# Kernel optimization log

Measured on AMD Instinct MI355X. Metric: run time of the kernel, lower is better.

## Reference

```python
import jax, jax.numpy as jnp
import numpy as np

OBS_LEN = 20
PRED_LEN = 30
NUM_MODES = 6
DATA_DIM = 2
DROPOUT_P = 0.25
NEG_SLOPE = 0.01
H_DIM = 256
B = 8192


def setup_inputs() -> dict:
    key = jax.random.key(0)
    ks = jax.random.split(key, 20)
    s = 0.05
    inp = {
        "traj_abs": jax.random.normal(ks[0], (OBS_LEN, B, DATA_DIM), jnp.float32),
        "traj_rel": jax.random.normal(ks[1], (OBS_LEN, B, DATA_DIM), jnp.float32),
        "state_h": jax.random.normal(ks[2], (1, B, H_DIM), jnp.float32),
        "c0": jax.random.normal(ks[3], (NUM_MODES, B, H_DIM), jnp.float32),
        # spatial embedding Linear(40, 40)
        "W_se": jax.random.normal(ks[4], (OBS_LEN * 2, OBS_LEN * 2), jnp.float32) * s,
        "b_se": jax.random.normal(ks[5], (OBS_LEN * 2,), jnp.float32) * s,
        # LSTM weights: input 40 -> hidden 256, gates order i,f,g,o
        "W_ih": jax.random.normal(ks[6], (4 * H_DIM, OBS_LEN * 2), jnp.float32) * s,
        "W_hh": jax.random.normal(ks[7], (4 * H_DIM, H_DIM), jnp.float32) * s,
        "b_ih": jax.random.normal(ks[8], (4 * H_DIM,), jnp.float32) * s,
        "b_hh": jax.random.normal(ks[9], (4 * H_DIM,), jnp.float32) * s,
        # per-mode prediction heads Linear(256, 2)
        "W_pred": jax.random.normal(ks[10], (NUM_MODES, DATA_DIM, H_DIM), jnp.float32) * s,
        "b_pred": jax.random.normal(ks[11], (NUM_MODES, DATA_DIM), jnp.float32) * s,
        # confidence PredictionNet (norm=False), latent = PRED_LEN*DATA_DIM = 60
        "pn_w1": jax.random.normal(ks[12], (PRED_LEN * DATA_DIM, PRED_LEN * DATA_DIM), jnp.float32) * s,
        "pn_b1": jax.random.normal(ks[13], (PRED_LEN * DATA_DIM,), jnp.float32) * s,
        "pn_w2": jax.random.normal(ks[14], (PRED_LEN * DATA_DIM, PRED_LEN * DATA_DIM), jnp.float32) * s,
        "pn_b2": jax.random.normal(ks[15], (PRED_LEN * DATA_DIM,), jnp.float32) * s,
        "pn_wfc": jax.random.normal(ks[16], (1, PRED_LEN * DATA_DIM), jnp.float32) * s,
        "pn_bfc": jax.random.normal(ks[17], (1,), jnp.float32) * s,
    }
    return inp


def _decode(traj_rel, state_h, c0, W_se, b_se, W_ih, W_hh, b_ih, b_hh,
            W_pred, b_pred, pn_w1, pn_b1, pn_w2, pn_b2, pn_wfc, pn_bfc):
    batch = traj_rel.shape[1]
    h0 = state_h[0]  # (B, H)
    keep = 1.0 - DROPOUT_P
    # one dropout key per (mode, step); deterministic stand-in for torch dropout
    keys = jax.random.split(jax.random.key(42), NUM_MODES * PRED_LEN).reshape(NUM_MODES, PRED_LEN)

    def one_mode(Wp, bp, c0m, keys_m):
        def step(carry, key):
            h, c, buf = carry  # buf: (OBS_LEN, B, 2) rolling window of rel displacements
            x = buf.transpose(1, 0, 2).reshape(batch, -1) @ W_se.T + b_se  # (B, 40)
            x = jnp.where(x > 0, x, NEG_SLOPE * x)  # leaky_relu
            mask = jax.random.bernoulli(key, keep, x.shape)
            x = jnp.where(mask, x / keep, 0.0)  # dropout (training=True)
            gates = x @ W_ih.T + b_ih + h @ W_hh.T + b_hh  # (B, 4H)
            i, f, g, o = jnp.split(gates, 4, axis=-1)
            c = jax.nn.sigmoid(f) * c + jax.nn.sigmoid(i) * jnp.tanh(g)
            h = jax.nn.sigmoid(o) * jnp.tanh(c)
            rel = h @ Wp.T + bp  # (B, 2)
            buf = jnp.roll(buf, -1, axis=0).at[-1].set(rel)
            return (h, c, buf), rel

        _, rels = jax.lax.scan(step, (h0, c0m, traj_rel), keys_m)
        return rels  # (PRED_LEN, B, 2)

    rels = jax.vmap(one_mode)(W_pred, b_pred, c0, keys)  # (M, T, B, 2)
    pred = rels.transpose(2, 0, 1, 3)  # (B, M, T, 2)

    # confidence PredictionNet (norm=False)
    x = pred.reshape(batch, NUM_MODES, PRED_LEN * DATA_DIM)
    y = jax.nn.relu(x @ pn_w1.T + pn_b1)
    y = jax.nn.relu(y @ pn_w2.T + pn_b2 + x)
    conf = (y @ pn_wfc.T + pn_bfc).reshape(batch, NUM_MODES)
    conf = jax.nn.softmax(conf, axis=1)
    return pred, conf


def reference(traj_abs, traj_rel, state_h, c0, W_se, b_se, W_ih, W_hh, b_ih, b_hh,
              W_pred, b_pred, pn_w1, pn_b1, pn_w2, pn_b2, pn_wfc, pn_bfc):
    # traj_abs unused in the 'Latent' branch (only its shape is read)
    return _decode(traj_rel, state_h, c0, W_se, b_se, W_ih, W_hh, b_ih, b_hh,
                   W_pred, b_pred, pn_w1, pn_b1, pn_w2, pn_b2, pn_wfc, pn_bfc)
```

## Files before the change

### kernel.cpp

```cpp
#include <hip/hip_runtime.h>
#include <cstdint>

#define JAX_PARTITIONABLE 1

#define OBS_LEN 20
#define PRED_LEN 30
#define NUM_MODES 6
#define BATCH 8192
#define H 256
#define MB (NUM_MODES * BATCH)
#define KPAD 320

typedef __attribute__((ext_vector_type(8))) short bf16x8;
typedef __attribute__((ext_vector_type(4))) float f32x4;

__host__ __device__ inline void tf2x32(uint32_t k0, uint32_t k1, uint32_t c0, uint32_t c1,
                                       uint32_t& o0, uint32_t& o1) {
  uint32_t ks0 = k0, ks1 = k1, ks2 = k0 ^ k1 ^ 0x1BD11BDAu;
  uint32_t x0 = c0 + ks0, x1 = c1 + ks1;
#define TF_R(x, r) (((x) << (r)) | ((x) >> (32 - (r))))
#define TF_RND(r)  { x0 += x1; x1 = TF_R(x1, r); x1 ^= x0; }
  TF_RND(13) TF_RND(15) TF_RND(26) TF_RND(6)   x0 += ks1; x1 += ks2 + 1u;
  TF_RND(17) TF_RND(29) TF_RND(16) TF_RND(24)  x0 += ks2; x1 += ks0 + 2u;
  TF_RND(13) TF_RND(15) TF_RND(26) TF_RND(6)   x0 += ks0; x1 += ks1 + 3u;
  TF_RND(17) TF_RND(29) TF_RND(16) TF_RND(24)  x0 += ks1; x1 += ks2 + 4u;
  TF_RND(13) TF_RND(15) TF_RND(26) TF_RND(6)   x0 += ks2; x1 += ks0 + 5u;
  o0 = x0; o1 = x1;
#undef TF_RND
#undef TF_R
}

__device__ inline void step_key(int m, int t, uint32_t& k0, uint32_t& k1) {
#if JAX_PARTITIONABLE
  tf2x32(0u, 42u, 0u, (uint32_t)(m * PRED_LEN + t), k0, k1);
#else
  int i = m * PRED_LEN + t;
  int n0 = 2 * i, n1 = 2 * i + 1;
  uint32_t a0, a1;
  if (n0 < 180) { tf2x32(0u, 42u, (uint32_t)n0, (uint32_t)(n0 + 180), a0, a1); k0 = a0; }
  else          { tf2x32(0u, 42u, (uint32_t)(n0 - 180), (uint32_t)n0, a0, a1); k0 = a1; }
  if (n1 < 180) { tf2x32(0u, 42u, (uint32_t)n1, (uint32_t)(n1 + 180), a0, a1); k1 = a0; }
  else          { tf2x32(0u, 42u, (uint32_t)(n1 - 180), (uint32_t)n1, a0, a1); k1 = a1; }
#endif
}

__device__ inline uint32_t mask_bits(uint32_t k0, uint32_t k1, uint32_t n) {
#if JAX_PARTITIONABLE
  uint32_t o0, o1;
  tf2x32(k0, k1, 0u, n, o0, o1);
  return o0 ^ o1;
#else
  const uint32_t HALF = (uint32_t)(BATCH * 40 / 2);
  uint32_t o0, o1;
  if (n < HALF) { tf2x32(k0, k1, n, n + HALF, o0, o1); return o0; }
  else          { tf2x32(k0, k1, n - HALF, n, o0, o1); return o1; }
#endif
}

__device__ __forceinline__ float sigf(float x) { return 1.0f / (1.0f + __expf(-x)); }
__device__ __forceinline__ float tanhfast(float x) {
  float e = __expf(-2.0f * fabsf(x));
  float t = (1.0f - e) / (1.0f + e);
  return x >= 0.f ? t : -t;
}
__device__ __forceinline__ ushort f2bf(float f) {
  uint32_t u = __float_as_uint(f);
  uint32_t r = (u + 0x7fffu + ((u >> 16) & 1u)) >> 16;
  return (ushort)r;
}
__device__ __forceinline__ float bf2f(uint32_t u) { return __uint_as_float(u << 16); }

__global__ __launch_bounds__(256) void k_prep(const float* __restrict__ Wih, const float* __restrict__ Whh,
                                              const float* __restrict__ bih, const float* __restrict__ bhh,
                                              ushort* __restrict__ WTb, float* __restrict__ bias) {
  int idx = blockIdx.x * 256 + threadIdx.x;
  if (idx < 1024 * KPAD) {
    int np = idx / KPAD, k = idx - np * KPAD;
    int cg = np >> 7, r = np & 127;
    int nt = r >> 4, col = r & 15;
    int N = (nt & 3) * 256 + cg * 32 + (nt >> 2) * 16 + col;
    float v = (k < 40) ? Wih[N * 40 + k] : (k < 296 ? Whh[N * 256 + (k - 40)] : 0.f);
    WTb[idx] = f2bf(v);
  }
  if (idx < 1024) bias[idx] = bih[idx] + bhh[idx];
}

__global__ __launch_bounds__(256) void k_init(const float* __restrict__ state_h, const float* __restrict__ c0,
                                              float* __restrict__ cst, ushort* __restrict__ Ab0,
                                              ushort* __restrict__ Ab1) {
  int idx = blockIdx.x * 256 + threadIdx.x;
  if (idx < MB * 64) {
    int row = idx >> 6;
    int j4 = (idx & 63) << 2;
    float4 cv = *(const float4*)(c0 + (size_t)idx * 4);
    *(float4*)(cst + (size_t)idx * 4) = cv;
    int b = row & (BATCH - 1);
    float4 hv = *(const float4*)(state_h + (size_t)b * H + j4);
    ushort4 hb = {f2bf(hv.x), f2bf(hv.y), f2bf(hv.z), f2bf(hv.w)};
    *(ushort4*)(Ab0 + (size_t)row * KPAD + 40 + j4) = hb;
  }
  if (idx < MB * 6) {
    int row = idx / 6, p4 = (idx - row * 6) << 2;
    ushort4 z = {0, 0, 0, 0};
    *(ushort4*)(Ab0 + (size_t)row * KPAD + 296 + p4) = z;
    *(ushort4*)(Ab1 + (size_t)row * KPAD + 296 + p4) = z;
  }
}

__global__ __launch_bounds__(256) void k_embed(const float* __restrict__ traj_rel, const float* __restrict__ rels,
                                               const float* __restrict__ Wse, const float* __restrict__ bse,
                                               ushort* __restrict__ Ax, int t) {
  __shared__ float sW[1600];
  __shared__ float sb[40];
  int tid = threadIdx.x;
  for (int i = tid; i < 1600; i += 256) sW[i] = Wse[i];
  if (tid < 40) sb[tid] = bse[tid];
  __syncthreads();
  int gid = blockIdx.x * 256 + tid;
  int b = gid & (BATCH - 1);
  int m = gid >> 13;
  float win[40];
#pragma unroll
  for (int kk = 0; kk < OBS_LEN; kk++) {
    int st = t + kk;
    const float* p = (st < OBS_LEN)
        ? (traj_rel + (((size_t)st * BATCH + b) << 1))
        : (rels + (((size_t)(m * PRED_LEN + (st - OBS_LEN)) * BATCH + b) << 1));
    float2 w = *(const float2*)p;
    win[kk * 2] = w.x; win[kk * 2 + 1] = w.y;
  }
  uint32_t k0, k1;
  step_key(m, t, k0, k1);
  uint32_t nb = (uint32_t)(b * 40);
  ushort* orow = Ax + (size_t)gid * KPAD;
#pragma unroll
  for (int jo = 0; jo < 5; jo++) {
    uint32_t pk[4];
#pragma unroll
    for (int jp = 0; jp < 4; jp++) {
      ushort lo = 0, hi = 0;
#pragma unroll
      for (int ji = 0; ji < 2; ji++) {
        int j = jo * 8 + jp * 2 + ji;
        float a = sb[j];
#pragma unroll
        for (int p = 0; p < 40; p += 4) {
          float4 w = *(const float4*)&sW[j * 40 + p];
          a = fmaf(win[p + 3], w.w, fmaf(win[p + 2], w.z, fmaf(win[p + 1], w.y, fmaf(win[p], w.x, a))));
        }
        a = a > 0.f ? a : 0.01f * a;
        uint32_t bits = mask_bits(k0, k1, nb + (uint32_t)j);
        float u = __uint_as_float((bits >> 9) | 0x3f800000u) - 1.0f;
        ushort r = (u < 0.75f) ? f2bf(a * 1.3333333730697632f) : (ushort)0;
        if (ji == 0) lo = r; else hi = r;
      }
      pk[jp] = (uint32_t)lo | ((uint32_t)hi << 16);
    }
    uint4 v = {pk[0], pk[1], pk[2], pk[3]};
    *(uint4*)(orow + jo * 8) = v;
  }
}

__global__ __launch_bounds__(256) void k_gates(const ushort* __restrict__ Ain, const ushort* __restrict__ WTb,
                                               const float* __restrict__ bias, float* __restrict__ cst,
                                               ushort* __restrict__ Anext) {
  __shared__ __align__(16) ushort lA[2][128][40];
  __shared__ __align__(16) ushort lB[2][128][40];
  int tid = threadIdx.x;
  int w = tid >> 6, lane = tid & 63;
  int row0 = blockIdx.x * 128;
  int cg = blockIdx.y;
  int sr = tid >> 1, sh = (tid & 1) << 4;
  const ushort* gA = Ain + (size_t)(row0 + sr) * KPAD + sh;
  const ushort* gB = WTb + (size_t)(cg * 128 + sr) * KPAD + sh;

  f32x4 zero = {0.f, 0.f, 0.f, 0.f};
  f32x4 acc[2][8];
#pragma unroll
  for (int i = 0; i < 2; i++)
#pragma unroll
    for (int j = 0; j < 8; j++) acc[i][j] = zero;

  uint4 ra0 = *(const uint4*)gA;
  uint4 ra1 = *(const uint4*)(gA + 8);
  uint4 rb0 = *(const uint4*)gB;
  uint4 rb1 = *(const uint4*)(gB + 8);
  *(uint4*)&lA[0][sr][sh] = ra0;
  *(uint4*)&lA[0][sr][sh + 8] = ra1;
  *(uint4*)&lB[0][sr][sh] = rb0;
  *(uint4*)&lB[0][sr][sh + 8] = rb1;
  __syncthreads();

  int fm = lane & 15, fq = lane >> 4;
  for (int kt = 0; kt < 10; kt++) {
    int cur = kt & 1;
    if (kt < 9) {
      ra0 = *(const uint4*)(gA + (kt + 1) * 32);
      ra1 = *(const uint4*)(gA + (kt + 1) * 32 + 8);
      rb0 = *(const uint4*)(gB + (kt + 1) * 32);
      rb1 = *(const uint4*)(gB + (kt + 1) * 32 + 8);
    }
    bf16x8 af[2], bfr[8];
#pragma unroll
    for (int rt = 0; rt < 2; rt++) af[rt] = *(const bf16x8*)&lA[cur][w * 32 + rt * 16 + fm][fq * 8];
#pragma unroll
    for (int nt = 0; nt < 8; nt++) bfr[nt] = *(const bf16x8*)&lB[cur][nt * 16 + fm][fq * 8];
#pragma unroll
    for (int rt = 0; rt < 2; rt++)
#pragma unroll
      for (int nt = 0; nt < 8; nt++)
        acc[rt][nt] = __builtin_amdgcn_mfma_f32_16x16x32_bf16(af[rt], bfr[nt], acc[rt][nt], 0, 0, 0);
    if (kt < 9) {
      *(uint4*)&lA[cur ^ 1][sr][sh] = ra0;
      *(uint4*)&lA[cur ^ 1][sr][sh + 8] = ra1;
      *(uint4*)&lB[cur ^ 1][sr][sh] = rb0;
      *(uint4*)&lB[cur ^ 1][sr][sh + 8] = rb1;
      __syncthreads();
    }
  }

#pragma unroll
  for (int jg = 0; jg < 2; jg++) {
    int jh = cg * 32 + jg * 16 + fm;
    float bi = bias[jh], bfg = bias[256 + jh], bg = bias[512 + jh], bo = bias[768 + jh];
#pragma unroll
    for (int rt = 0; rt < 2; rt++) {
#pragma unroll
      for (int reg = 0; reg < 4; reg++) {
        int row = row0 + w * 32 + rt * 16 + fq * 4 + reg;
        float gi = acc[rt][jg * 4 + 0][reg] + bi;
        float gf = acc[rt][jg * 4 + 1][reg] + bfg;
        float gg = acc[rt][jg * 4 + 2][reg] + bg;
        float go = acc[rt][jg * 4 + 3][reg] + bo;
        size_t ci = (size_t)row * H + jh;
        float cv = cst[ci];
        float c2 = sigf(gf) * cv + sigf(gi) * tanhfast(gg);
        cst[ci] = c2;
        float hn = sigf(go) * tanhfast(c2);
        Anext[(size_t)row * KPAD + 40 + jh] = f2bf(hn);
      }
    }
  }
}

__global__ __launch_bounds__(256) void k_pred(const ushort* __restrict__ hsrc, const float* __restrict__ Wp,
                                              const float* __restrict__ bp, float* __restrict__ rels, int t) {
  int tid = threadIdx.x;
  int wv = tid >> 6, lane = tid & 63;
  int grp = lane >> 3, lg = lane & 7;
  int row = blockIdx.x * 32 + wv * 8 + grp;
  int m = row / BATCH, b = row & (BATCH - 1);
  const ushort* hr = hsrc + (size_t)row * KPAD + 40 + lg * 32;
  const float* w0 = Wp + m * 512 + lg * 32;
  const float* w1 = w0 + 256;
  float s0 = 0.f, s1 = 0.f;
#pragma unroll
  for (int q = 0; q < 4; q++) {
    uint4 hv = *(const uint4*)(hr + q * 8);
    float h0 = bf2f(hv.x & 0xffffu), h1 = bf2f(hv.x >> 16);
    float h2 = bf2f(hv.y & 0xffffu), h3 = bf2f(hv.y >> 16);
    float h4 = bf2f(hv.z & 0xffffu), h5 = bf2f(hv.z >> 16);
    float h6 = bf2f(hv.w & 0xffffu), h7 = bf2f(hv.w >> 16);
    float4 wa0 = *(const float4*)(w0 + q * 8);
    float4 wa1 = *(const float4*)(w0 + q * 8 + 4);
    float4 wb0 = *(const float4*)(w1 + q * 8);
    float4 wb1 = *(const float4*)(w1 + q * 8 + 4);
    s0 += h0 * wa0.x + h1 * wa0.y + h2 * wa0.z + h3 * wa0.w
        + h4 * wa1.x + h5 * wa1.y + h6 * wa1.z + h7 * wa1.w;
    s1 += h0 * wb0.x + h1 * wb0.y + h2 * wb0.z + h3 * wb0.w
        + h4 * wb1.x + h5 * wb1.y + h6 * wb1.z + h7 * wb1.w;
  }
#pragma unroll
  for (int off = 1; off < 8; off <<= 1) {
    s0 += __shfl_xor(s0, off, 64);
    s1 += __shfl_xor(s1, off, 64);
  }
  if (lg == 0) {
    float2 r = make_float2(s0 + bp[m * 2], s1 + bp[m * 2 + 1]);
    *(float2*)(rels + ((size_t)(m * PRED_LEN + t) * BATCH + b) * 2) = r;
  }
}

__global__ __launch_bounds__(256) void k_transconf(const float* __restrict__ rels,
                                                   const float* __restrict__ W1, const float* __restrict__ b1,
                                                   const float* __restrict__ W2, const float* __restrict__ b2,
                                                   const float* __restrict__ wfc, const float* __restrict__ bfc,
                                                   float* __restrict__ out) {
  __shared__ float tile[32][361];
  __shared__ float sW1[3600];
  __shared__ float sW2[3600];
  __shared__ float sb1[60], sb2[60], swfc[60];
  __shared__ float sy1[192][61];
  __shared__ float slg[32][6];
  int tid = threadIdx.x;
  for (int i = tid; i < 3600; i += 256) { sW1[i] = W1[i]; sW2[i] = W2[i]; }
  if (tid < 60) { sb1[tid] = b1[tid]; sb2[tid] = b2[tid]; swfc[tid] = wfc[tid]; }
  int b0 = blockIdx.x * 32;
  for (int i = tid; i < 11520; i += 256) {
    int bl = i & 31, c = i >> 5;
    int mm = c / 60, r = c % 60;
    tile[bl][c] = rels[((size_t)((mm * PRED_LEN + (r >> 1)) * BATCH) + (b0 + bl)) * 2 + (r & 1)];
  }
  __syncthreads();
  for (int i = tid; i < 11520; i += 256) {
    int bl = i / 360, c = i % 360;
    out[(size_t)(b0 + bl) * 360 + c] = tile[bl][c];
  }
  if (tid < 192) {
    int bl = tid / 6, mm = tid - bl * 6;
    int xb = mm * 60;
    for (int q = 0; q < 60; q++) {
      float acl = sb1[q];
#pragma unroll
      for (int p = 0; p < 60; p++) acl = fmaf(tile[bl][xb + p], sW1[q * 60 + p], acl);
      sy1[tid][q] = fmaxf(acl, 0.f);
    }
    float logit = bfc[0];
    for (int q = 0; q < 60; q++) {
      float acl = sb2[q] + tile[bl][xb + q];
#pragma unroll
      for (int p = 0; p < 60; p++) acl = fmaf(sy1[tid][p], sW2[q * 60 + p], acl);
      logit = fmaf(fmaxf(acl, 0.f), swfc[q], logit);
    }
    slg[bl][mm] = logit;
  }
  __syncthreads();
  if (tid < 32) {
    float mx = slg[tid][0];
#pragma unroll
    for (int m = 1; m < 6; m++) mx = fmaxf(mx, slg[tid][m]);
    float e[6], s = 0.f;
#pragma unroll
    for (int m = 0; m < 6; m++) { e[m] = __expf(slg[tid][m] - mx); s += e[m]; }
    float inv = 1.0f / s;
    size_t base = (size_t)BATCH * 360 + (size_t)(b0 + tid) * 6;
#pragma unroll
    for (int m = 0; m < 6; m++) out[base + m] = e[m] * inv;
  }
}

extern "C" void kernel_launch(void* const* d_in, const int* in_sizes, int n_in,
                              void* d_out, int out_size, void* d_ws, size_t ws_size,
                              hipStream_t stream) {
  const float* traj_rel = (const float*)d_in[1];
  const float* state_h  = (const float*)d_in[2];
  const float* c0       = (const float*)d_in[3];
  const float* Wse      = (const float*)d_in[4];
  const float* bse      = (const float*)d_in[5];
  const float* Wih      = (const float*)d_in[6];
  const float* Whh      = (const float*)d_in[7];
  const float* bih      = (const float*)d_in[8];
  const float* bhh      = (const float*)d_in[9];
  const float* Wp       = (const float*)d_in[10];
  const float* bp       = (const float*)d_in[11];
  const float* W1       = (const float*)d_in[12];
  const float* b1       = (const float*)d_in[13];
  const float* W2       = (const float*)d_in[14];
  const float* b2       = (const float*)d_in[15];
  const float* wfc      = (const float*)d_in[16];
  const float* bfc      = (const float*)d_in[17];
  float* out = (float*)d_out;

  float* cst  = (float*)d_ws;
  float* rels = cst + (size_t)MB * H;
  float* bias = rels + (size_t)NUM_MODES * PRED_LEN * BATCH * 2;
  ushort* WTb = (ushort*)(bias + 1024);
  ushort* Ab0 = WTb + (size_t)1024 * KPAD;
  ushort* Ab1 = Ab0 + (size_t)MB * KPAD;

  k_prep<<<1280, 256, 0, stream>>>(Wih, Whh, bih, bhh, WTb, bias);
  k_init<<<12288, 256, 0, stream>>>(state_h, c0, cst, Ab0, Ab1);
  for (int t = 0; t < PRED_LEN; t++) {
    ushort* Acur  = (t & 1) ? Ab1 : Ab0;
    ushort* Anext = (t & 1) ? Ab0 : Ab1;
    k_embed<<<192, 256, 0, stream>>>(traj_rel, rels, Wse, bse, Acur, t);
    k_gates<<<dim3(384, 8), 256, 0, stream>>>(Acur, WTb, bias, cst, Anext);
    k_pred<<<1536, 256, 0, stream>>>(Anext, Wp, bp, rels, t);
  }
  k_transconf<<<256, 256, 0, stream>>>(rels, W1, b1, W2, b2, wfc, bfc, out);
}
```

Baseline: 3.525 ms.

## Fuse whole 30-step LSTM decode into one persistent kernel with on-chip state

Replaces the per-step embed/gates/pred launches (90 launches) with one kernel where each block owns 64 rows of one mode and loops over all 30 steps. Cell state stays in registers, hidden state and the input window stay in LDS, and the gate GEMM uses 32x32x16 bf16 MFMA with weights pre-swizzled and streamed from global/L2 each step. This removes the global round-trips of h, c and the A matrix plus launch overhead. In exchange it depends on occupancy of 768 blocks of 512 threads with large register/LDS use, and re-reads the full weight matrix per block per step from cache.

```diff
diff --git a/kernel.cpp b/kernel.cpp
--- a/kernel.cpp
+++ b/kernel.cpp
@@ -9,10 +9,9 @@
 #define BATCH 8192
 #define H 256
 #define MB (NUM_MODES * BATCH)
-#define KPAD 320
 
 typedef __attribute__((ext_vector_type(8))) short bf16x8;
-typedef __attribute__((ext_vector_type(4))) float f32x4;
+typedef __attribute__((ext_vector_type(16))) float f32x16;
 
 __host__ __device__ inline void tf2x32(uint32_t k0, uint32_t k1, uint32_t c0, uint32_t c1,
                                        uint32_t& o0, uint32_t& o1) {
@@ -71,213 +70,198 @@
 __device__ __forceinline__ float bf2f(uint32_t u) { return __uint_as_float(u << 16); }
 
 __global__ __launch_bounds__(256) void k_prep(const float* __restrict__ Wih, const float* __restrict__ Whh,
-                                              const float* __restrict__ bih, const float* __restrict__ bhh,
-                                              ushort* __restrict__ WTb, float* __restrict__ bias) {
+                                              ushort* __restrict__ W2) {
   int idx = blockIdx.x * 256 + threadIdx.x;
-  if (idx < 1024 * KPAD) {
-    int np = idx / KPAD, k = idx - np * KPAD;
-    int cg = np >> 7, r = np & 127;
-    int nt = r >> 4, col = r & 15;
-    int N = (nt & 3) * 256 + cg * 32 + (nt >> 2) * 16 + col;
+  if (idx < 20 * 8 * 4 * 2 * 32 * 8) {
+    int j = idx & 7, n = (idx >> 3) & 31, kh = (idx >> 8) & 1;
+    int g = (idx >> 9) & 3, w = (idx >> 11) & 7, kt = idx >> 14;
+    int N = g * 256 + w * 32 + n;
+    int k = kt * 16 + kh * 8 + j;
     float v = (k < 40) ? Wih[N * 40 + k] : (k < 296 ? Whh[N * 256 + (k - 40)] : 0.f);
-    WTb[idx] = f2bf(v);
-  }
-  if (idx < 1024) bias[idx] = bih[idx] + bhh[idx];
-}
-
-__global__ __launch_bounds__(256) void k_init(const float* __restrict__ state_h, const float* __restrict__ c0,
-                                              float* __restrict__ cst, ushort* __restrict__ Ab0,
-                                              ushort* __restrict__ Ab1) {
-  int idx = blockIdx.x * 256 + threadIdx.x;
-  if (idx < MB * 64) {
-    int row = idx >> 6;
-    int j4 = (idx & 63) << 2;
-    float4 cv = *(const float4*)(c0 + (size_t)idx * 4);
-    *(float4*)(cst + (size_t)idx * 4) = cv;
-    int b = row & (BATCH - 1);
-    float4 hv = *(const float4*)(state_h + (size_t)b * H + j4);
-    ushort4 hb = {f2bf(hv.x), f2bf(hv.y), f2bf(hv.z), f2bf(hv.w)};
-    *(ushort4*)(Ab0 + (size_t)row * KPAD + 40 + j4) = hb;
-  }
-  if (idx < MB * 6) {
-    int row = idx / 6, p4 = (idx - row * 6) << 2;
-    ushort4 z = {0, 0, 0, 0};
-    *(ushort4*)(Ab0 + (size_t)row * KPAD + 296 + p4) = z;
-    *(ushort4*)(Ab1 + (size_t)row * KPAD + 296 + p4) = z;
-  }
-}
-
-__global__ __launch_bounds__(256) void k_embed(const float* __restrict__ traj_rel, const float* __restrict__ rels,
-                                               const float* __restrict__ Wse, const float* __restrict__ bse,
-                                               ushort* __restrict__ Ax, int t) {
-  __shared__ float sW[1600];
-  __shared__ float sb[40];
+    W2[idx] = f2bf(v);
+  }
+}
+
+__global__ __launch_bounds__(512, 2) void k_decode(
+    const float* __restrict__ traj_rel, const float* __restrict__ state_h,
+    const float* __restrict__ c0, const float* __restrict__ Wse, const float* __restrict__ bse,
+    const float* __restrict__ bih, const float* __restrict__ bhh,
+    const ushort* __restrict__ W2, const float* __restrict__ Wp, const float* __restrict__ bp,
+    float* __restrict__ rels) {
+  __shared__ __align__(16) ushort sA[64][328];
+  __shared__ float sWse[1600];
+  __shared__ float sWp[512];
+  __shared__ float sbse[40];
+  __shared__ float swin[64][40];
+
   int tid = threadIdx.x;
-  for (int i = tid; i < 1600; i += 256) sW[i] = Wse[i];
-  if (tid < 40) sb[tid] = bse[tid];
+  int w = tid >> 6, lane = tid & 63;
+  int khl = lane >> 5, col = lane & 31;
+  int blk = blockIdx.x;
+  int m = blk >> 7;
+  int b0 = (blk & 127) * 64;
+  int jh = w * 32 + col;
+
+  for (int i = tid; i < 1600; i += 512) sWse[i] = Wse[i];
+  if (tid < 512) sWp[tid] = Wp[m * 512 + tid];
+  if (tid < 40) sbse[tid] = bse[tid];
+  for (int i = tid; i < 64 * 20; i += 512) {
+    int row = i / 20, kk = i - row * 20;
+    float2 v = *(const float2*)(traj_rel + ((size_t)kk * BATCH + b0 + row) * 2);
+    swin[row][kk * 2] = v.x; swin[row][kk * 2 + 1] = v.y;
+  }
+  for (int i = tid; i < 64 * 256; i += 512) {
+    int row = i >> 8, j = i & 255;
+    sA[row][40 + j] = f2bf(state_h[((size_t)(b0 + row)) * 256 + j]);
+  }
+  for (int i = tid; i < 64 * 32; i += 512) {
+    int row = i >> 5;
+    sA[row][296 + (i & 31)] = 0;
+  }
+  float rbi = bih[jh] + bhh[jh];
+  float rbf = bih[256 + jh] + bhh[256 + jh];
+  float rbg = bih[512 + jh] + bhh[512 + jh];
+  float rbo = bih[768 + jh] + bhh[768 + jh];
+  float creg[2][16];
+#pragma unroll
+  for (int rt = 0; rt < 2; rt++)
+#pragma unroll
+    for (int reg = 0; reg < 16; reg++) {
+      int row = rt * 32 + (reg & 3) + 8 * (reg >> 2) + 4 * khl;
+      creg[rt][reg] = c0[((size_t)m * BATCH + b0 + row) * H + jh];
+    }
+  float bpx = bp[m * 2], bpy = bp[m * 2 + 1];
   __syncthreads();
-  int gid = blockIdx.x * 256 + tid;
-  int b = gid & (BATCH - 1);
-  int m = gid >> 13;
-  float win[40];
-#pragma unroll
-  for (int kk = 0; kk < OBS_LEN; kk++) {
-    int st = t + kk;
-    const float* p = (st < OBS_LEN)
-        ? (traj_rel + (((size_t)st * BATCH + b) << 1))
-        : (rels + (((size_t)(m * PRED_LEN + (st - OBS_LEN)) * BATCH + b) << 1));
-    float2 w = *(const float2*)p;
-    win[kk * 2] = w.x; win[kk * 2 + 1] = w.y;
-  }
-  uint32_t k0, k1;
-  step_key(m, t, k0, k1);
-  uint32_t nb = (uint32_t)(b * 40);
-  ushort* orow = Ax + (size_t)gid * KPAD;
-#pragma unroll
-  for (int jo = 0; jo < 5; jo++) {
-    uint32_t pk[4];
-#pragma unroll
-    for (int jp = 0; jp < 4; jp++) {
-      ushort lo = 0, hi = 0;
-#pragma unroll
-      for (int ji = 0; ji < 2; ji++) {
-        int j = jo * 8 + jp * 2 + ji;
-        float a = sb[j];
+
+  int q = tid & 7, prow = tid >> 3;
+  const int jb0 = q * 32;
+
+#pragma unroll 1
+  for (int t = 0; t < PRED_LEN; t++) {
+    if (t > 0) {
+      float s0 = 0.f, s1 = 0.f;
+#pragma unroll
+      for (int p = 0; p < 4; p++) {
+        uint4 hv = *(const uint4*)&sA[prow][40 + jb0 + p * 8];
+        float hh[8] = {bf2f(hv.x & 0xffffu), bf2f(hv.x >> 16), bf2f(hv.y & 0xffffu), bf2f(hv.y >> 16),
+                       bf2f(hv.z & 0xffffu), bf2f(hv.z >> 16), bf2f(hv.w & 0xffffu), bf2f(hv.w >> 16)};
+#pragma unroll
+        for (int e = 0; e < 8; e++) {
+          s0 = fmaf(hh[e], sWp[jb0 + p * 8 + e], s0);
+          s1 = fmaf(hh[e], sWp[256 + jb0 + p * 8 + e], s1);
+        }
+      }
+#pragma unroll
+      for (int off = 1; off < 8; off <<= 1) {
+        s0 += __shfl_xor(s0, off, 64);
+        s1 += __shfl_xor(s1, off, 64);
+      }
+      if (q == 0) {
+        float rx = s0 + bpx, ry = s1 + bpy;
+        *(float2*)(rels + ((size_t)(m * PRED_LEN + (t - 1)) * BATCH + b0 + prow) * 2) =
+            make_float2(rx, ry);
+        int slot = (t - 1) % 20;
+        swin[prow][slot * 2] = rx; swin[prow][slot * 2 + 1] = ry;
+      }
+    }
+    {
+      uint32_t k0, k1;
+      step_key(m, t, k0, k1);
+      float win[40];
+#pragma unroll
+      for (int kk = 0; kk < 20; kk++) {
+        int idx = t + kk;
+        if (idx >= 40) idx -= 40; else if (idx >= 20) idx -= 20;
+        win[kk * 2] = swin[prow][idx * 2];
+        win[kk * 2 + 1] = swin[prow][idx * 2 + 1];
+      }
+      uint32_t nb = (uint32_t)((b0 + prow) * 40 + q * 5);
+#pragma unroll
+      for (int jj = 0; jj < 5; jj++) {
+        int j = q * 5 + jj;
+        float a = sbse[j];
 #pragma unroll
         for (int p = 0; p < 40; p += 4) {
-          float4 w = *(const float4*)&sW[j * 40 + p];
-          a = fmaf(win[p + 3], w.w, fmaf(win[p + 2], w.z, fmaf(win[p + 1], w.y, fmaf(win[p], w.x, a))));
+          float4 wv = *(const float4*)&sWse[j * 40 + p];
+          a = fmaf(win[p + 3], wv.w, fmaf(win[p + 2], wv.z, fmaf(win[p + 1], wv.y, fmaf(win[p], wv.x, a))));
         }
         a = a > 0.f ? a : 0.01f * a;
-        uint32_t bits = mask_bits(k0, k1, nb + (uint32_t)j);
+        uint32_t bits = mask_bits(k0, k1, nb + (uint32_t)jj);
         float u = __uint_as_float((bits >> 9) | 0x3f800000u) - 1.0f;
-        ushort r = (u < 0.75f) ? f2bf(a * 1.3333333730697632f) : (ushort)0;
-        if (ji == 0) lo = r; else hi = r;
-      }
-      pk[jp] = (uint32_t)lo | ((uint32_t)hi << 16);
-    }
-    uint4 v = {pk[0], pk[1], pk[2], pk[3]};
-    *(uint4*)(orow + jo * 8) = v;
-  }
-}
-
-__global__ __launch_bounds__(256) void k_gates(const ushort* __restrict__ Ain, const ushort* __restrict__ WTb,
-                                               const float* __restrict__ bias, float* __restrict__ cst,
-                                               ushort* __restrict__ Anext) {
-  __shared__ __align__(16) ushort lA[2][128][40];
-  __shared__ __align__(16) ushort lB[2][128][40];
-  int tid = threadIdx.x;
-  int w = tid >> 6, lane = tid & 63;
-  int row0 = blockIdx.x * 128;
-  int cg = blockIdx.y;
-  int sr = tid >> 1, sh = (tid & 1) << 4;
-  const ushort* gA = Ain + (size_t)(row0 + sr) * KPAD + sh;
-  const ushort* gB = WTb + (size_t)(cg * 128 + sr) * KPAD + sh;
-
-  f32x4 zero = {0.f, 0.f, 0.f, 0.f};
-  f32x4 acc[2][8];
-#pragma unroll
-  for (int i = 0; i < 2; i++)
-#pragma unroll
-    for (int j = 0; j < 8; j++) acc[i][j] = zero;
-
-  uint4 ra0 = *(const uint4*)gA;
-  uint4 ra1 = *(const uint4*)(gA + 8);
-  uint4 rb0 = *(const uint4*)gB;
-  uint4 rb1 = *(const uint4*)(gB + 8);
-  *(uint4*)&lA[0][sr][sh] = ra0;
-  *(uint4*)&lA[0][sr][sh + 8] = ra1;
-  *(uint4*)&lB[0][sr][sh] = rb0;
-  *(uint4*)&lB[0][sr][sh + 8] = rb1;
-  __syncthreads();
-
-  int fm = lane & 15, fq = lane >> 4;
-  for (int kt = 0; kt < 10; kt++) {
-    int cur = kt & 1;
-    if (kt < 9) {
-      ra0 = *(const uint4*)(gA + (kt + 1) * 32);
-      ra1 = *(const uint4*)(gA + (kt + 1) * 32 + 8);
-      rb0 = *(const uint4*)(gB + (kt + 1) * 32);
-      rb1 = *(const uint4*)(gB + (kt + 1) * 32 + 8);
-    }
-    bf16x8 af[2], bfr[8];
-#pragma unroll
-    for (int rt = 0; rt < 2; rt++) af[rt] = *(const bf16x8*)&lA[cur][w * 32 + rt * 16 + fm][fq * 8];
-#pragma unroll
-    for (int nt = 0; nt < 8; nt++) bfr[nt] = *(const bf16x8*)&lB[cur][nt * 16 + fm][fq * 8];
+        sA[prow][j] = (u < 0.75f) ? f2bf(a * 1.3333333730697632f) : (ushort)0;
+      }
+    }
+    __syncthreads();
+
+    f32x16 acc[2][4];
 #pragma unroll
     for (int rt = 0; rt < 2; rt++)
 #pragma unroll
-      for (int nt = 0; nt < 8; nt++)
-        acc[rt][nt] = __builtin_amdgcn_mfma_f32_16x16x32_bf16(af[rt], bfr[nt], acc[rt][nt], 0, 0, 0);
-    if (kt < 9) {
-      *(uint4*)&lA[cur ^ 1][sr][sh] = ra0;
-      *(uint4*)&lA[cur ^ 1][sr][sh + 8] = ra1;
-      *(uint4*)&lB[cur ^ 1][sr][sh] = rb0;
-      *(uint4*)&lB[cur ^ 1][sr][sh + 8] = rb1;
-      __syncthreads();
-    }
-  }
-
-#pragma unroll
-  for (int jg = 0; jg < 2; jg++) {
-    int jh = cg * 32 + jg * 16 + fm;
-    float bi = bias[jh], bfg = bias[256 + jh], bg = bias[512 + jh], bo = bias[768 + jh];
-#pragma unroll
-    for (int rt = 0; rt < 2; rt++) {
-#pragma unroll
-      for (int reg = 0; reg < 4; reg++) {
-        int row = row0 + w * 32 + rt * 16 + fq * 4 + reg;
-        float gi = acc[rt][jg * 4 + 0][reg] + bi;
-        float gf = acc[rt][jg * 4 + 1][reg] + bfg;
-        float gg = acc[rt][jg * 4 + 2][reg] + bg;
-        float go = acc[rt][jg * 4 + 3][reg] + bo;
-        size_t ci = (size_t)row * H + jh;
-        float cv = cst[ci];
-        float c2 = sigf(gf) * cv + sigf(gi) * tanhfast(gg);
-        cst[ci] = c2;
-        float hn = sigf(go) * tanhfast(c2);
-        Anext[(size_t)row * KPAD + 40 + jh] = f2bf(hn);
-      }
-    }
-  }
-}
-
-__global__ __launch_bounds__(256) void k_pred(const ushort* __restrict__ hsrc, const float* __restrict__ Wp,
-                                              const float* __restrict__ bp, float* __restrict__ rels, int t) {
-  int tid = threadIdx.x;
-  int wv = tid >> 6, lane = tid & 63;
-  int grp = lane >> 3, lg = lane & 7;
-  int row = blockIdx.x * 32 + wv * 8 + grp;
-  int m = row / BATCH, b = row & (BATCH - 1);
-  const ushort* hr = hsrc + (size_t)row * KPAD + 40 + lg * 32;
-  const float* w0 = Wp + m * 512 + lg * 32;
-  const float* w1 = w0 + 256;
-  float s0 = 0.f, s1 = 0.f;
-#pragma unroll
-  for (int q = 0; q < 4; q++) {
-    uint4 hv = *(const uint4*)(hr + q * 8);
-    float h0 = bf2f(hv.x & 0xffffu), h1 = bf2f(hv.x >> 16);
-    float h2 = bf2f(hv.y & 0xffffu), h3 = bf2f(hv.y >> 16);
-    float h4 = bf2f(hv.z & 0xffffu), h5 = bf2f(hv.z >> 16);
-    float h6 = bf2f(hv.w & 0xffffu), h7 = bf2f(hv.w >> 16);
-    float4 wa0 = *(const float4*)(w0 + q * 8);
-    float4 wa1 = *(const float4*)(w0 + q * 8 + 4);
-    float4 wb0 = *(const float4*)(w1 + q * 8);
-    float4 wb1 = *(const float4*)(w1 + q * 8 + 4);
-    s0 += h0 * wa0.x + h1 * wa0.y + h2 * wa0.z + h3 * wa0.w
-        + h4 * wa1.x + h5 * wa1.y + h6 * wa1.z + h7 * wa1.w;
-    s1 += h0 * wb0.x + h1 * wb0.y + h2 * wb0.z + h3 * wb0.w
-        + h4 * wb1.x + h5 * wb1.y + h6 * wb1.z + h7 * wb1.w;
-  }
-#pragma unroll
-  for (int off = 1; off < 8; off <<= 1) {
-    s0 += __shfl_xor(s0, off, 64);
-    s1 += __shfl_xor(s1, off, 64);
-  }
-  if (lg == 0) {
-    float2 r = make_float2(s0 + bp[m * 2], s1 + bp[m * 2 + 1]);
-    *(float2*)(rels + ((size_t)(m * PRED_LEN + t) * BATCH + b) * 2) = r;
+      for (int g = 0; g < 4; g++)
+#pragma unroll
+        for (int reg = 0; reg < 16; reg++) acc[rt][g][reg] = 0.f;
+
+    const ushort* Wbase = W2 + (size_t)lane * 8;
+    bf16x8 bc[4], bn[4];
+#pragma unroll
+    for (int g = 0; g < 4; g++) bc[g] = *(const bf16x8*)(Wbase + ((0 * 8 + w) * 4 + g) * 512);
+#pragma unroll
+    for (int kt = 0; kt < 20; kt++) {
+      if (kt < 19) {
+#pragma unroll
+        for (int g = 0; g < 4; g++)
+          bn[g] = *(const bf16x8*)(Wbase + (((kt + 1) * 8 + w) * 4 + g) * 512);
+      }
+      bf16x8 a0 = *(const bf16x8*)&sA[col][kt * 16 + khl * 8];
+      bf16x8 a1 = *(const bf16x8*)&sA[32 + col][kt * 16 + khl * 8];
+#pragma unroll
+      for (int g = 0; g < 4; g++) {
+        acc[0][g] = __builtin_amdgcn_mfma_f32_32x32x16_bf16(a0, bc[g], acc[0][g], 0, 0, 0);
+        acc[1][g] = __builtin_amdgcn_mfma_f32_32x32x16_bf16(a1, bc[g], acc[1][g], 0, 0, 0);
+      }
+#pragma unroll
+      for (int g = 0; g < 4; g++) bc[g] = bn[g];
+    }
+    __syncthreads();
+
+#pragma unroll
+    for (int rt = 0; rt < 2; rt++)
+#pragma unroll
+      for (int reg = 0; reg < 16; reg++) {
+        int row = rt * 32 + (reg & 3) + 8 * (reg >> 2) + 4 * khl;
+        float gi = acc[rt][0][reg] + rbi;
+        float gf = acc[rt][1][reg] + rbf;
+        float gg = acc[rt][2][reg] + rbg;
+        float go = acc[rt][3][reg] + rbo;
+        float c2 = sigf(gf) * creg[rt][reg] + sigf(gi) * tanhfast(gg);
+        creg[rt][reg] = c2;
+        sA[row][40 + jh] = f2bf(sigf(go) * tanhfast(c2));
+      }
+    __syncthreads();
+  }
+
+  {
+    float s0 = 0.f, s1 = 0.f;
+#pragma unroll
+    for (int p = 0; p < 4; p++) {
+      uint4 hv = *(const uint4*)&sA[prow][40 + jb0 + p * 8];
+      float hh[8] = {bf2f(hv.x & 0xffffu), bf2f(hv.x >> 16), bf2f(hv.y & 0xffffu), bf2f(hv.y >> 16),
+                     bf2f(hv.z & 0xffffu), bf2f(hv.z >> 16), bf2f(hv.w & 0xffffu), bf2f(hv.w >> 16)};
+#pragma unroll
+      for (int e = 0; e < 8; e++) {
+        s0 = fmaf(hh[e], sWp[jb0 + p * 8 + e], s0);
+        s1 = fmaf(hh[e], sWp[256 + jb0 + p * 8 + e], s1);
+      }
+    }
+#pragma unroll
+    for (int off = 1; off < 8; off <<= 1) {
+      s0 += __shfl_xor(s0, off, 64);
+      s1 += __shfl_xor(s1, off, 64);
+    }
+    if (q == 0) {
+      *(float2*)(rels + ((size_t)(m * PRED_LEN + 29) * BATCH + b0 + prow) * 2) =
+          make_float2(s0 + bpx, s1 + bpy);
+    }
   }
 }
 
@@ -309,18 +293,18 @@
   if (tid < 192) {
     int bl = tid / 6, mm = tid - bl * 6;
     int xb = mm * 60;
-    for (int q = 0; q < 60; q++) {
-      float acl = sb1[q];
-#pragma unroll
-      for (int p = 0; p < 60; p++) acl = fmaf(tile[bl][xb + p], sW1[q * 60 + p], acl);
-      sy1[tid][q] = fmaxf(acl, 0.f);
+    for (int qq = 0; qq < 60; qq++) {
+      float acl = sb1[qq];
+#pragma unroll
+      for (int p = 0; p < 60; p++) acl = fmaf(tile[bl][xb + p], sW1[qq * 60 + p], acl);
+      sy1[tid][qq] = fmaxf(acl, 0.f);
     }
     float logit = bfc[0];
-    for (int q = 0; q < 60; q++) {
-      float acl = sb2[q] + tile[bl][xb + q];
-#pragma unroll
-      for (int p = 0; p < 60; p++) acl = fmaf(sy1[tid][p], sW2[q * 60 + p], acl);
-      logit = fmaf(fmaxf(acl, 0.f), swfc[q], logit);
+    for (int qq = 0; qq < 60; qq++) {
+      float acl = sb2[qq] + tile[bl][xb + qq];
+#pragma unroll
+      for (int p = 0; p < 60; p++) acl = fmaf(sy1[tid][p], sW2[qq * 60 + p], acl);
+      logit = fmaf(fmaxf(acl, 0.f), swfc[qq], logit);
     }
     slg[bl][mm] = logit;
   }
@@ -328,14 +312,14 @@
   if (tid < 32) {
     float mx = slg[tid][0];
 #pragma unroll
-    for (int m = 1; m < 6; m++) mx = fmaxf(mx, slg[tid][m]);
+    for (int mm = 1; mm < 6; mm++) mx = fmaxf(mx, slg[tid][mm]);
     float e[6], s = 0.f;
 #pragma unroll
-    for (int m = 0; m < 6; m++) { e[m] = __expf(slg[tid][m] - mx); s += e[m]; }
+    for (int mm = 0; mm < 6; mm++) { e[mm] = __expf(slg[tid][mm] - mx); s += e[mm]; }
     float inv = 1.0f / s;
     size_t base = (size_t)BATCH * 360 + (size_t)(b0 + tid) * 6;
 #pragma unroll
-    for (int m = 0; m < 6; m++) out[base + m] = e[m] * inv;
+    for (int mm = 0; mm < 6; mm++) out[base + mm] = e[mm] * inv;
   }
 }
 
@@ -355,27 +339,17 @@
   const float* bp       = (const float*)d_in[11];
   const float* W1       = (const float*)d_in[12];
   const float* b1       = (const float*)d_in[13];
-  const float* W2       = (const float*)d_in[14];
+  const float* W2c      = (const float*)d_in[14];
   const float* b2       = (const float*)d_in[15];
   const float* wfc      = (const float*)d_in[16];
   const float* bfc      = (const float*)d_in[17];
   float* out = (float*)d_out;
 
-  float* cst  = (float*)d_ws;
-  float* rels = cst + (size_t)MB * H;
-  float* bias = rels + (size_t)NUM_MODES * PRED_LEN * BATCH * 2;
-  ushort* WTb = (ushort*)(bias + 1024);
-  ushort* Ab0 = WTb + (size_t)1024 * KPAD;
-  ushort* Ab1 = Ab0 + (size_t)MB * KPAD;
-
-  k_prep<<<1280, 256, 0, stream>>>(Wih, Whh, bih, bhh, WTb, bias);
-  k_init<<<12288, 256, 0, stream>>>(state_h, c0, cst, Ab0, Ab1);
-  for (int t = 0; t < PRED_LEN; t++) {
-    ushort* Acur  = (t & 1) ? Ab1 : Ab0;
-    ushort* Anext = (t & 1) ? Ab0 : Ab1;
-    k_embed<<<192, 256, 0, stream>>>(traj_rel, rels, Wse, bse, Acur, t);
-    k_gates<<<dim3(384, 8), 256, 0, stream>>>(Acur, WTb, bias, cst, Anext);
-    k_pred<<<1536, 256, 0, stream>>>(Anext, Wp, bp, rels, t);
-  }
-  k_transconf<<<256, 256, 0, stream>>>(rels, W1, b1, W2, b2, wfc, bfc, out);
-}
+  float* rels = (float*)d_ws;
+  ushort* W2  = (ushort*)(rels + (size_t)NUM_MODES * PRED_LEN * BATCH * 2);
+
+  k_prep<<<1280, 256, 0, stream>>>(Wih, Whh, W2);
+  k_decode<<<768, 512, 0, stream>>>(traj_rel, state_h, c0, Wse, bse, bih, bhh,
+                                    W2, Wp, bp, rels);
+  k_transconf<<<256, 256, 0, stream>>>(rels, W1, b1, W2c, b2, wfc, bfc, out);
+}
```

Result: slower. 4.663 ms (+32.3%).
